# Optimization experiments

Hardware: AMD Instinct MI355X
Metric: run time of the kernel (lower is better)

## Reference

```python
import jax, jax.numpy as jnp
import numpy as np

# Model dims (match init_kwargs)
E, D, H, K = 8, 512, 1024, 2   # num_experts, input/output dim, hidden dim, top_k
B, S = 4, 2048                 # batch, seq_len


def setup_inputs() -> dict:
    key = jax.random.key(0)
    ks = jax.random.split(key, 5)
    sd = lambda fan: np.float32(1.0 / np.sqrt(fan))
    return {
        "x": jax.random.normal(ks[0], (B, S, D), jnp.float32),
        "gate_w": jax.random.normal(ks[1], (D, E), jnp.float32) * sd(D),
        "gate_b": jnp.zeros((E,), jnp.float32),
        "w1": jax.random.normal(ks[2], (E, D, H), jnp.float32) * sd(D),
        "b1": jnp.zeros((E, H), jnp.float32),
        "w2": jax.random.normal(ks[3], (E, H, D), jnp.float32) * sd(H),
        "b2": jnp.zeros((E, D), jnp.float32),
    }


def reference(x, gate_w, gate_b, w1, b1, w2, b2):
    # x: [B, S, D]
    Bb, Ss, Dd = x.shape
    xf = x.reshape(-1, Dd)                              # [N, D], N = B*S

    # Router: softmax over experts, top-k, renormalize selected weights
    logits = xf @ gate_w + gate_b                        # [N, E]
    probs = jax.nn.softmax(logits, axis=-1)              # [N, E]
    top_w, top_i = jax.lax.top_k(probs, K)               # [N, K]
    top_w = top_w / top_w.sum(axis=-1, keepdims=True)

    # Per-token combine weight for each expert (0 if not routed).
    onehot = jax.nn.one_hot(top_i, E, dtype=probs.dtype)  # [N, K, E]
    combine = jnp.einsum("nke,nk->ne", onehot, top_w)     # [N, E]

    # Expert MLPs. Dropout is inactive at inference (identity).
    # h: [E, N, H]; GELU exact (torch nn.GELU default uses erf)
    h = jax.nn.gelu(jnp.einsum("nd,edh->enh", xf, w1) + b1[:, None, :],
                    approximate=False)
    y = jnp.einsum("enh,ehd->end", h, w2) + b2[:, None, :]  # [E, N, D]

    # Weighted combine: tokens not routed to expert e have combine[:, e] == 0.
    out = jnp.einsum("end,ne->nd", y, combine).reshape(Bb, Ss, Dd)
    return out, probs.reshape(Bb, Ss, E)
```

## Files before the change

### kernel.cpp

```cpp
#include <hip/hip_runtime.h>
#include <stdint.h>

#define N_TOK 8192
#define DIM   512
#define HID   1024
#define NE    8
#define NSLOT 16384
#define MAXSLOT 17408

typedef __attribute__((ext_vector_type(8))) short short8;
typedef __attribute__((ext_vector_type(4))) float f32x4;

#define W1T_OFF  0ull
#define W2T_OFF  8388608ull
#define H_OFF    16777216ull
#define Y_OFF    52428800ull
#define XBF_OFF  52428800ull
#define TOPI_OFF 70254592ull
#define TOPW_OFF 70320128ull
#define SLOT_OFF 70385664ull
#define ROWS_OFF 70451200ull
#define RW_OFF   70520832ull
#define CNT_OFF  70590464ull

__device__ __forceinline__ unsigned int f2bfu(float f) {
  union { float f; unsigned int i; } v; v.f = f;
  unsigned int u = v.i;
  return (u + 0x7FFFu + ((u >> 16) & 1u)) >> 16;
}
__device__ __forceinline__ float bf2f(unsigned int u) {
  union { unsigned int i; float f; } v; v.i = (u & 0xFFFFu) << 16; return v.f;
}
__device__ __forceinline__ float gelu_f(float x) {
  float x2 = x * x;
  float u = x * (1.59576912f + 0.07135481f * x2);
  float ez = __expf(-u);
  return x * __builtin_amdgcn_rcpf(1.0f + ez);
}
__device__ __forceinline__ void async16(void* lds, const void* g) {
  __builtin_amdgcn_global_load_lds(
      (const __attribute__((address_space(1))) unsigned int*)g,
      (__attribute__((address_space(3))) unsigned int*)lds, 16, 0, 0);
}

__global__ __launch_bounds__(256) void k_prep(
    const float* __restrict__ w1, const float* __restrict__ w2,
    unsigned short* __restrict__ w1t, unsigned short* __restrict__ w2t,
    const float* __restrict__ x, const float* __restrict__ gw,
    const float* __restrict__ gb, float* __restrict__ probs_out,
    int2* __restrict__ topi, float2* __restrict__ topw,
    unsigned short* __restrict__ xbf) {
  __shared__ unsigned short tile[64][68];
  int tid = threadIdx.x;
  if (blockIdx.x < 2048) {
    int b = blockIdx.x;
    const float* src; unsigned short* dst; int R, C;
    if (b < 1024) { int e = b >> 7; int t = b & 127;
      src = w1 + (size_t)e * 524288; dst = w1t + (size_t)e * 524288; R = 512; C = 1024;
      int tr = t >> 4, tc = t & 15;
      src += (size_t)tr * 64 * C + tc * 64; dst += (size_t)tc * 64 * R + tr * 64;
    } else { b -= 1024; int e = b >> 7; int t = b & 127;
      src = w2 + (size_t)e * 524288; dst = w2t + (size_t)e * 524288; R = 1024; C = 512;
      int tr = t >> 3, tc = t & 7;
      src += (size_t)tr * 64 * C + tc * 64; dst += (size_t)tc * 64 * R + tr * 64;
    }
#pragma unroll
    for (int i = 0; i < 4; ++i) {
      int l = i * 256 + tid;
      int r = l >> 4, c4 = (l & 15) << 2;
      float4 v = *(const float4*)(src + (size_t)r * C + c4);
      tile[r][c4 + 0] = (unsigned short)f2bfu(v.x);
      tile[r][c4 + 1] = (unsigned short)f2bfu(v.y);
      tile[r][c4 + 2] = (unsigned short)f2bfu(v.z);
      tile[r][c4 + 3] = (unsigned short)f2bfu(v.w);
    }
    __syncthreads();
#pragma unroll
    for (int i = 0; i < 2; ++i) {
      int l = i * 256 + tid;
      int rr = l >> 3, c8 = (l & 7) << 3;
      ushort4 a, b2v;
      a.x = tile[c8 + 0][rr]; a.y = tile[c8 + 1][rr];
      a.z = tile[c8 + 2][rr]; a.w = tile[c8 + 3][rr];
      b2v.x = tile[c8 + 4][rr]; b2v.y = tile[c8 + 5][rr];
      b2v.z = tile[c8 + 6][rr]; b2v.w = tile[c8 + 7][rr];
      uint4 pk;
      pk.x = (unsigned int)a.x | ((unsigned int)a.y << 16);
      pk.y = (unsigned int)a.z | ((unsigned int)a.w << 16);
      pk.z = (unsigned int)b2v.x | ((unsigned int)b2v.y << 16);
      pk.w = (unsigned int)b2v.z | ((unsigned int)b2v.w << 16);
      *(uint4*)(dst + (size_t)rr * R + c8) = pk;
    }
  } else {
    int wave = tid >> 6, lane = tid & 63;
    int n = (blockIdx.x - 2048) * 4 + wave;
    const float4* xr = (const float4*)(x + (size_t)n * DIM);
    float4 x0 = xr[lane * 2], x1 = xr[lane * 2 + 1];
    float xf[8] = {x0.x, x0.y, x0.z, x0.w, x1.x, x1.y, x1.z, x1.w};
    uint4 pa;
    pa.x = f2bfu(xf[0]) | (f2bfu(xf[1]) << 16);
    pa.y = f2bfu(xf[2]) | (f2bfu(xf[3]) << 16);
    pa.z = f2bfu(xf[4]) | (f2bfu(xf[5]) << 16);
    pa.w = f2bfu(xf[6]) | (f2bfu(xf[7]) << 16);
    *(uint4*)(xbf + (size_t)n * DIM + lane * 8) = pa;
    float acc[8] = {0.f,0.f,0.f,0.f,0.f,0.f,0.f,0.f};
    const float4* gwr = (const float4*)gw;
#pragma unroll
    for (int j = 0; j < 8; ++j) {
      int d = lane * 8 + j;
      float4 g0 = gwr[d * 2], g1 = gwr[d * 2 + 1];
      acc[0] += xf[j] * g0.x; acc[1] += xf[j] * g0.y; acc[2] += xf[j] * g0.z; acc[3] += xf[j] * g0.w;
      acc[4] += xf[j] * g1.x; acc[5] += xf[j] * g1.y; acc[6] += xf[j] * g1.z; acc[7] += xf[j] * g1.w;
    }
#pragma unroll
    for (int o = 1; o < 64; o <<= 1)
#pragma unroll
      for (int e = 0; e < 8; ++e) acc[e] += __shfl_xor(acc[e], o, 64);
    float p[8], mx = -1e30f, s = 0.f;
#pragma unroll
    for (int e = 0; e < 8; ++e) { p[e] = acc[e] + gb[e]; mx = fmaxf(mx, p[e]); }
#pragma unroll
    for (int e = 0; e < 8; ++e) { p[e] = __expf(p[e] - mx); s += p[e]; }
    float inv = 1.f / s;
#pragma unroll
    for (int e = 0; e < 8; ++e) p[e] *= inv;
    if (lane < 8) probs_out[(size_t)n * NE + lane] = p[lane];
    if (lane == 0) {
      int i0 = 0; float v0 = p[0];
#pragma unroll
      for (int e = 1; e < 8; ++e) if (p[e] > v0) { v0 = p[e]; i0 = e; }
      int i1 = -1; float v1 = -1.f;
#pragma unroll
      for (int e = 0; e < 8; ++e) if (e != i0 && p[e] > v1) { v1 = p[e]; i1 = e; }
      float sw = 1.f / (v0 + v1);
      topi[n] = make_int2(i0, i1);
      topw[n] = make_float2(v0 * sw, v1 * sw);
    }
  }
}

__global__ __launch_bounds__(1024) void k_countassign(
    const int2* __restrict__ topi, const float2* __restrict__ topw,
    int* __restrict__ meta, int* __restrict__ rows, float* __restrict__ rw,
    int* __restrict__ slot_of) {
  __shared__ int ch[32][8];
  __shared__ int tot[8], poff_s[9], tiles_s[8];
  __shared__ int sm_off[1024 * 8];
  int t = threadIdx.x, g = t >> 5;
  if (t < 256) ((int*)ch)[t] = 0;
  __syncthreads();
  int2 te[8]; float2 tw[8];
  int c[8] = {0,0,0,0,0,0,0,0};
  int base_tok = t * 8;
#pragma unroll
  for (int i = 0; i < 8; ++i) {
    te[i] = topi[base_tok + i];
    tw[i] = topw[base_tok + i];
#pragma unroll
    for (int k = 0; k < 8; ++k) c[k] += (te[i].x == k) + (te[i].y == k);
  }
#pragma unroll
  for (int k = 0; k < 8; ++k) if (c[k]) atomicAdd(&ch[g][k], c[k]);
#pragma unroll
  for (int k = 0; k < 8; ++k) {
    int s = c[k];
#pragma unroll
    for (int d = 1; d < 32; d <<= 1) {
      int u = __shfl_up(s, d, 32);
      if ((t & 31) >= d) s += u;
    }
    sm_off[t * 8 + k] = s - c[k];
  }
  __syncthreads();
  if (t < 8) {
    int a = 0;
#pragma unroll
    for (int b = 0; b < 32; ++b) { int v = ch[b][t]; ch[b][t] = a; a += v; }
    tot[t] = a; meta[t] = a;
  }
  __syncthreads();
  if (t == 0) {
    int a = 0, ts = 0;
#pragma unroll
    for (int e = 0; e < 8; ++e) {
      int tiles = (tot[e] + 127) >> 7;
      poff_s[e] = a; tiles_s[e] = tiles;
      meta[16 + e] = a; meta[32 + e] = ts;
      a += tiles << 7; ts += tiles;
    }
    poff_s[8] = a; meta[24] = a; meta[40] = ts;
  }
  __syncthreads();
#pragma unroll
  for (int i = 0; i < 8; ++i) {
    int n = base_tok + i;
    int e0 = te[i].x, e1 = te[i].y;
    int o0 = sm_off[t * 8 + e0]++;
    int s0 = poff_s[e0] + ch[g][e0] + o0;
    int o1 = sm_off[t * 8 + e1]++;
    int s1 = poff_s[e1] + ch[g][e1] + o1;
    rows[s0] = n; rw[s0] = tw[i].x; slot_of[2 * n] = s0;
    rows[s1] = n; rw[s1] = tw[i].y; slot_of[2 * n + 1] = s1;
  }
#pragma unroll
  for (int e = 0; e < 8; ++e) {
    int padn = (tiles_s[e] << 7) - tot[e];
    if (t < padn) {
      int s = poff_s[e] + tot[e] + t;
      rows[s] = 0; rw[s] = 0.f;
    }
  }
}

__global__ __launch_bounds__(256) void k_gemm1(
    const unsigned short* __restrict__ xbf, const unsigned short* __restrict__ w1t,
    const float* __restrict__ b1, const int* __restrict__ meta,
    const int* __restrict__ rows, unsigned short* __restrict__ h) {
  int lin = blockIdx.x;
  int xcd = lin & 7, j = lin >> 3;
  int t = xcd * 17 + (j >> 3);
  int nt = j & 7;
  if (t >= meta[40]) return;
  int e = 0;
#pragma unroll
  for (int i = 1; i < 8; ++i) if (t >= meta[32 + i]) e = i;
  int mt = t - meta[32 + e];
  int row0 = meta[16 + e] + (mt << 7);
  __shared__ __align__(16) unsigned short As[2][8192];
  __shared__ __align__(16) unsigned short Bs[2][8192];
  int tid = threadIdx.x;
  int wave = tid >> 6, lane = tid & 63;
  int wr = wave & 1, wc = wave >> 1;
  int ml = lane & 15, q = lane >> 4;
  f32x4 acc[4][4] = {};
  const unsigned short* bBase = w1t + (size_t)e * HID * DIM + (size_t)(nt * 128) * DIM;

  const unsigned short* ga[4]; const unsigned short* gb[4];
#pragma unroll
  for (int jj = 0; jj < 4; ++jj) {
    int s = jj * 256 + tid;
    int ks = s >> 9, r = (s >> 2) & 127, cs = s & 3;
    int col = ks * 32 + ((cs ^ ((r >> 1) & 3)) << 3);
    ga[jj] = xbf + (size_t)rows[row0 + r] * DIM + col;
    gb[jj] = bBase + (size_t)r * DIM + col;
  }

#define STAGE1(buf, k0) do { \
    _Pragma("unroll") \
    for (int jj = 0; jj < 4; ++jj) { \
      int dst = (jj * 256 + wave * 64) * 8; \
      async16(&As[buf][dst], ga[jj] + (k0)); \
      async16(&Bs[buf][dst], gb[jj] + (k0)); \
    } \
  } while (0)

  STAGE1(0, 0);
  __syncthreads();

  for (int k0 = 0; k0 < DIM; k0 += 64) {
    int cur = (k0 >> 6) & 1, nxt = cur ^ 1;
    if (k0 + 64 < DIM) STAGE1(nxt, k0 + 64);
#pragma unroll
    for (int ks = 0; ks < 2; ++ks) {
      short8 tf[4], wf[4];
#pragma unroll
      for (int am = 0; am < 4; ++am) {
        int ra = wr * 64 + am * 16 + ml;
        tf[am] = *(const short8*)&As[cur][ks * 4096 + (ra * 4 + (q ^ ((ra >> 1) & 3))) * 8];
      }
#pragma unroll
      for (int an = 0; an < 4; ++an) {
        int rb = wc * 64 + an * 16 + ml;
        wf[an] = *(const short8*)&Bs[cur][ks * 4096 + (rb * 4 + (q ^ ((rb >> 1) & 3))) * 8];
      }
#pragma unroll
      for (int an = 0; an < 4; ++an)
#pragma unroll
        for (int am = 0; am < 4; ++am)
          acc[an][am] = __builtin_amdgcn_mfma_f32_16x16x32_bf16(wf[an], tf[am], acc[an][am], 0, 0, 0);
    }
    __syncthreads();
  }
#undef STAGE1

#pragma unroll
  for (int am = 0; am < 4; ++am) {
    int slot_r = row0 + wr * 64 + am * 16 + ml;
    unsigned short* hrow = h + (size_t)slot_r * HID;
#pragma unroll
    for (int an = 0; an < 4; ++an) {
      int colb = nt * 128 + wc * 64 + an * 16 + q * 4;
      float4 bias = *(const float4*)&b1[e * HID + colb];
      f32x4 v = acc[an][am];
      float g0 = gelu_f(v[0] + bias.x);
      float g1 = gelu_f(v[1] + bias.y);
      float g2 = gelu_f(v[2] + bias.z);
      float g3 = gelu_f(v[3] + bias.w);
      uint2 pk;
      pk.x = f2bfu(g0) | (f2bfu(g1) << 16);
      pk.y = f2bfu(g2) | (f2bfu(g3) << 16);
      *(uint2*)(hrow + colb) = pk;
    }
  }
}

__global__ __launch_bounds__(256) void k_gemm2(
    const unsigned short* __restrict__ h, const unsigned short* __restrict__ w2t,
    const float* __restrict__ b2, const int* __restrict__ meta,
    const float* __restrict__ rw, unsigned short* __restrict__ y) {
  int lin = blockIdx.x;
  int xcd = lin & 7, j = lin >> 3;
  int t = xcd * 17 + (j >> 2);
  int nt = j & 3;
  if (t >= meta[40]) return;
  int e = 0;
#pragma unroll
  for (int i = 1; i < 8; ++i) if (t >= meta[32 + i]) e = i;
  int mt = t - meta[32 + e];
  int row0 = meta[16 + e] + (mt << 7);
  __shared__ __align__(16) unsigned short As[2][8192];
  __shared__ __align__(16) unsigned short Bs[2][8192];
  int tid = threadIdx.x;
  int wave = tid >> 6, lane = tid & 63;
  int wr = wave & 1, wc = wave >> 1;
  int ml = lane & 15, q = lane >> 4;
  f32x4 acc[4][4] = {};
  const unsigned short* aBase = h + (size_t)row0 * HID;
  const unsigned short* bBase = w2t + (size_t)e * DIM * HID + (size_t)(nt * 128) * HID;

  const unsigned short* ga[4]; const unsigned short* gb[4];
#pragma unroll
  for (int jj = 0; jj < 4; ++jj) {
    int s = jj * 256 + tid;
    int ks = s >> 9, r = (s >> 2) & 127, cs = s & 3;
    int col = ks * 32 + ((cs ^ ((r >> 1) & 3)) << 3);
    ga[jj] = aBase + (size_t)r * HID + col;
    gb[jj] = bBase + (size_t)r * HID + col;
  }

#define STAGE2(buf, k0) do { \
    _Pragma("unroll") \
    for (int jj = 0; jj < 4; ++jj) { \
      int dst = (jj * 256 + wave * 64) * 8; \
      async16(&As[buf][dst], ga[jj] + (k0)); \
      async16(&Bs[buf][dst], gb[jj] + (k0)); \
    } \
  } while (0)

  STAGE2(0, 0);
  __syncthreads();

  for (int k0 = 0; k0 < HID; k0 += 64) {
    int cur = (k0 >> 6) & 1, nxt = cur ^ 1;
    if (k0 + 64 < HID) STAGE2(nxt, k0 + 64);
#pragma unroll
    for (int ks = 0; ks < 2; ++ks) {
      short8 tf[4], wf[4];
#pragma unroll
      for (int am = 0; am < 4; ++am) {
        int ra = wr * 64 + am * 16 + ml;
        tf[am] = *(const short8*)&As[cur][ks * 4096 + (ra * 4 + (q ^ ((ra >> 1) & 3))) * 8];
      }
#pragma unroll
      for (int an = 0; an < 4; ++an) {
        int rb = wc * 64 + an * 16 + ml;
        wf[an] = *(const short8*)&Bs[cur][ks * 4096 + (rb * 4 + (q ^ ((rb >> 1) & 3))) * 8];
      }
#pragma unroll
      for (int an = 0; an < 4; ++an)
#pragma unroll
        for (int am = 0; am < 4; ++am)
          acc[an][am] = __builtin_amdgcn_mfma_f32_16x16x32_bf16(wf[an], tf[am], acc[an][am], 0, 0, 0);
    }
    __syncthreads();
  }
#undef STAGE2

#pragma unroll
  for (int am = 0; am < 4; ++am) {
    int slot_r = row0 + wr * 64 + am * 16 + ml;
    float w = rw[slot_r];
    unsigned short* yrow = y + (size_t)slot_r * DIM;
#pragma unroll
    for (int an = 0; an < 4; ++an) {
      int colb = nt * 128 + wc * 64 + an * 16 + q * 4;
      float4 bias = *(const float4*)&b2[e * DIM + colb];
      f32x4 v = acc[an][am];
      uint2 pk;
      pk.x = f2bfu((v[0] + bias.x) * w) | (f2bfu((v[1] + bias.y) * w) << 16);
      pk.y = f2bfu((v[2] + bias.z) * w) | (f2bfu((v[3] + bias.w) * w) << 16);
      *(uint2*)(yrow + colb) = pk;
    }
  }
}

__global__ __launch_bounds__(256) void k_combine(
    const unsigned short* __restrict__ y, const int* __restrict__ slot_of,
    float* __restrict__ out) {
  int t = blockIdx.x * 256 + threadIdx.x;
  int n = t >> 6, c = (t & 63) << 3;
  int s0 = slot_of[2 * n], s1 = slot_of[2 * n + 1];
  uint4 u0 = *(const uint4*)(y + (size_t)s0 * DIM + c);
  uint4 u1 = *(const uint4*)(y + (size_t)s1 * DIM + c);
  float4 o0, o1;
  o0.x = bf2f(u0.x) + bf2f(u1.x); o0.y = bf2f(u0.x >> 16) + bf2f(u1.x >> 16);
  o0.z = bf2f(u0.y) + bf2f(u1.y); o0.w = bf2f(u0.y >> 16) + bf2f(u1.y >> 16);
  o1.x = bf2f(u0.z) + bf2f(u1.z); o1.y = bf2f(u0.z >> 16) + bf2f(u1.z >> 16);
  o1.z = bf2f(u0.w) + bf2f(u1.w); o1.w = bf2f(u0.w >> 16) + bf2f(u1.w >> 16);
  *(float4*)(out + (size_t)n * DIM + c) = o0;
  *(float4*)(out + (size_t)n * DIM + c + 4) = o1;
}

extern "C" void kernel_launch(void* const* d_in, const int* in_sizes, int n_in,
                              void* d_out, int out_size, void* d_ws, size_t ws_size,
                              hipStream_t stream) {
  const float* x  = (const float*)d_in[0];
  const float* gw = (const float*)d_in[1];
  const float* gb = (const float*)d_in[2];
  const float* w1 = (const float*)d_in[3];
  const float* b1 = (const float*)d_in[4];
  const float* w2 = (const float*)d_in[5];
  const float* b2 = (const float*)d_in[6];
  float* out = (float*)d_out;
  char* ws = (char*)d_ws;

  unsigned short* w1t = (unsigned short*)(ws + W1T_OFF);
  unsigned short* w2t = (unsigned short*)(ws + W2T_OFF);
  unsigned short* h   = (unsigned short*)(ws + H_OFF);
  unsigned short* y   = (unsigned short*)(ws + Y_OFF);
  unsigned short* xbf = (unsigned short*)(ws + XBF_OFF);
  int2*   topi    = (int2*)(ws + TOPI_OFF);
  float2* topw    = (float2*)(ws + TOPW_OFF);
  int*    slot_of = (int*)(ws + SLOT_OFF);
  int*    rows    = (int*)(ws + ROWS_OFF);
  float*  rw      = (float*)(ws + RW_OFF);
  int*    meta    = (int*)(ws + CNT_OFF);
  float*  probs   = out + (size_t)N_TOK * DIM;

  k_prep       <<<dim3(4096), dim3(256),  0, stream>>>(w1, w2, w1t, w2t,
                                                       x, gw, gb, probs, topi, topw, xbf);
  k_countassign<<<dim3(1),    dim3(1024), 0, stream>>>(topi, topw, meta, rows, rw, slot_of);
  k_gemm1      <<<dim3(1088), dim3(256),  0, stream>>>(xbf, w1t, b1, meta, rows, h);
  k_gemm2      <<<dim3(544),  dim3(256),  0, stream>>>(h, w2t, b2, meta, rw, y);
  k_combine    <<<dim3(2048), dim3(256),  0, stream>>>(y, slot_of, out);
}
```

Baseline: 214.2 us.

## Enlarge expert GEMM M-tiles to 256 rows with 8 waves and K-step 32

Both expert GEMMs now use 256-row M tiles (per-expert padding to 256) with 512-thread blocks of 8 waves arranged 4x2, while the K step per stage drops from 64 to 32. Weight tiles are reused across more token rows, cutting global weight traffic, and LDS per block shrinks on the B side. The tradeoffs are more padding waste per expert, fewer blocks (less parallelism on a large GPU), and twice as many barriers per K loop. Workspace offsets are enlarged to fit the bigger padded slot count.

```diff
diff --git a/kernel.cpp b/kernel.cpp
--- a/kernel.cpp
+++ b/kernel.cpp
@@ -6,7 +6,7 @@
 #define HID   1024
 #define NE    8
 #define NSLOT 16384
-#define MAXSLOT 17408
+#define MAXSLOT 18432
 
 typedef __attribute__((ext_vector_type(8))) short short8;
 typedef __attribute__((ext_vector_type(4))) float f32x4;
@@ -14,14 +14,14 @@
 #define W1T_OFF  0ull
 #define W2T_OFF  8388608ull
 #define H_OFF    16777216ull
-#define Y_OFF    52428800ull
-#define XBF_OFF  52428800ull
-#define TOPI_OFF 70254592ull
-#define TOPW_OFF 70320128ull
-#define SLOT_OFF 70385664ull
-#define ROWS_OFF 70451200ull
-#define RW_OFF   70520832ull
-#define CNT_OFF  70590464ull
+#define Y_OFF    54525952ull
+#define XBF_OFF  54525952ull
+#define TOPI_OFF 73400320ull
+#define TOPW_OFF 73465856ull
+#define SLOT_OFF 73531392ull
+#define ROWS_OFF 73596928ull
+#define RW_OFF   73670656ull
+#define CNT_OFF  73744384ull
 
 __device__ __forceinline__ unsigned int f2bfu(float f) {
   union { float f; unsigned int i; } v; v.f = f;
@@ -183,10 +183,10 @@
     int a = 0, ts = 0;
 #pragma unroll
     for (int e = 0; e < 8; ++e) {
-      int tiles = (tot[e] + 127) >> 7;
+      int tiles = (tot[e] + 255) >> 8;
       poff_s[e] = a; tiles_s[e] = tiles;
       meta[16 + e] = a; meta[32 + e] = ts;
-      a += tiles << 7; ts += tiles;
+      a += tiles << 8; ts += tiles;
     }
     poff_s[8] = a; meta[24] = a; meta[40] = ts;
   }
@@ -204,7 +204,7 @@
   }
 #pragma unroll
   for (int e = 0; e < 8; ++e) {
-    int padn = (tiles_s[e] << 7) - tot[e];
+    int padn = (tiles_s[e] << 8) - tot[e];
     if (t < padn) {
       int s = poff_s[e] + tot[e] + t;
       rows[s] = 0; rw[s] = 0.f;
@@ -212,66 +212,65 @@
   }
 }
 
-__global__ __launch_bounds__(256) void k_gemm1(
+__global__ __launch_bounds__(512, 4) void k_gemm1(
     const unsigned short* __restrict__ xbf, const unsigned short* __restrict__ w1t,
     const float* __restrict__ b1, const int* __restrict__ meta,
     const int* __restrict__ rows, unsigned short* __restrict__ h) {
   int lin = blockIdx.x;
   int xcd = lin & 7, j = lin >> 3;
-  int t = xcd * 17 + (j >> 3);
+  int t = xcd * 9 + (j >> 3);
   int nt = j & 7;
   if (t >= meta[40]) return;
   int e = 0;
 #pragma unroll
   for (int i = 1; i < 8; ++i) if (t >= meta[32 + i]) e = i;
   int mt = t - meta[32 + e];
-  int row0 = meta[16 + e] + (mt << 7);
+  int row0 = meta[16 + e] + (mt << 8);
   __shared__ __align__(16) unsigned short As[2][8192];
-  __shared__ __align__(16) unsigned short Bs[2][8192];
+  __shared__ __align__(16) unsigned short Bs[2][4096];
   int tid = threadIdx.x;
   int wave = tid >> 6, lane = tid & 63;
-  int wr = wave & 1, wc = wave >> 1;
+  int wr = wave & 3, wc = wave >> 2;
   int ml = lane & 15, q = lane >> 4;
   f32x4 acc[4][4] = {};
   const unsigned short* bBase = w1t + (size_t)e * HID * DIM + (size_t)(nt * 128) * DIM;
 
-  const unsigned short* ga[4]; const unsigned short* gb[4];
-#pragma unroll
-  for (int jj = 0; jj < 4; ++jj) {
-    int s = jj * 256 + tid;
-    int ks = s >> 9, r = (s >> 2) & 127, cs = s & 3;
-    int col = ks * 32 + ((cs ^ ((r >> 1) & 3)) << 3);
-    ga[jj] = xbf + (size_t)rows[row0 + r] * DIM + col;
-    gb[jj] = bBase + (size_t)r * DIM + col;
-  }
+  const unsigned short *ga0, *ga1, *gbp;
+  {
+    int s0 = tid;        int r0 = s0 >> 2; int c0 = ((s0 & 3) ^ ((r0 >> 1) & 3)) << 3;
+    ga0 = xbf + (size_t)rows[row0 + r0] * DIM + c0;
+    int s1 = 512 + tid;  int r1 = s1 >> 2; int c1 = ((s1 & 3) ^ ((r1 >> 1) & 3)) << 3;
+    ga1 = xbf + (size_t)rows[row0 + r1] * DIM + c1;
+    int sb = tid;        int rb = sb >> 2; int cb = ((sb & 3) ^ ((rb >> 1) & 3)) << 3;
+    gbp = bBase + (size_t)rb * DIM + cb;
+  }
+  int la0 = (wave * 64) * 8;
+  int la1 = (512 + wave * 64) * 8;
+  int lb  = (wave * 64) * 8;
 
 #define STAGE1(buf, k0) do { \
-    _Pragma("unroll") \
-    for (int jj = 0; jj < 4; ++jj) { \
-      int dst = (jj * 256 + wave * 64) * 8; \
-      async16(&As[buf][dst], ga[jj] + (k0)); \
-      async16(&Bs[buf][dst], gb[jj] + (k0)); \
-    } \
+    async16(&As[buf][la0], ga0 + (k0)); \
+    async16(&As[buf][la1], ga1 + (k0)); \
+    async16(&Bs[buf][lb],  gbp + (k0)); \
   } while (0)
 
   STAGE1(0, 0);
   __syncthreads();
 
-  for (int k0 = 0; k0 < DIM; k0 += 64) {
-    int cur = (k0 >> 6) & 1, nxt = cur ^ 1;
-    if (k0 + 64 < DIM) STAGE1(nxt, k0 + 64);
-#pragma unroll
-    for (int ks = 0; ks < 2; ++ks) {
+  for (int k0 = 0; k0 < DIM; k0 += 32) {
+    int cur = (k0 >> 5) & 1, nxt = cur ^ 1;
+    if (k0 + 32 < DIM) STAGE1(nxt, k0 + 32);
+    {
       short8 tf[4], wf[4];
 #pragma unroll
       for (int am = 0; am < 4; ++am) {
         int ra = wr * 64 + am * 16 + ml;
-        tf[am] = *(const short8*)&As[cur][ks * 4096 + (ra * 4 + (q ^ ((ra >> 1) & 3))) * 8];
+        tf[am] = *(const short8*)&As[cur][(ra * 4 + (q ^ ((ra >> 1) & 3))) * 8];
       }
 #pragma unroll
       for (int an = 0; an < 4; ++an) {
         int rb = wc * 64 + an * 16 + ml;
-        wf[an] = *(const short8*)&Bs[cur][ks * 4096 + (rb * 4 + (q ^ ((rb >> 1) & 3))) * 8];
+        wf[an] = *(const short8*)&Bs[cur][(rb * 4 + (q ^ ((rb >> 1) & 3))) * 8];
       }
 #pragma unroll
       for (int an = 0; an < 4; ++an)
@@ -304,67 +303,66 @@
   }
 }
 
-__global__ __launch_bounds__(256) void k_gemm2(
+__global__ __launch_bounds__(512, 4) void k_gemm2(
     const unsigned short* __restrict__ h, const unsigned short* __restrict__ w2t,
     const float* __restrict__ b2, const int* __restrict__ meta,
     const float* __restrict__ rw, unsigned short* __restrict__ y) {
   int lin = blockIdx.x;
   int xcd = lin & 7, j = lin >> 3;
-  int t = xcd * 17 + (j >> 2);
+  int t = xcd * 9 + (j >> 2);
   int nt = j & 3;
   if (t >= meta[40]) return;
   int e = 0;
 #pragma unroll
   for (int i = 1; i < 8; ++i) if (t >= meta[32 + i]) e = i;
   int mt = t - meta[32 + e];
-  int row0 = meta[16 + e] + (mt << 7);
+  int row0 = meta[16 + e] + (mt << 8);
   __shared__ __align__(16) unsigned short As[2][8192];
-  __shared__ __align__(16) unsigned short Bs[2][8192];
+  __shared__ __align__(16) unsigned short Bs[2][4096];
   int tid = threadIdx.x;
   int wave = tid >> 6, lane = tid & 63;
-  int wr = wave & 1, wc = wave >> 1;
+  int wr = wave & 3, wc = wave >> 2;
   int ml = lane & 15, q = lane >> 4;
   f32x4 acc[4][4] = {};
   const unsigned short* aBase = h + (size_t)row0 * HID;
   const unsigned short* bBase = w2t + (size_t)e * DIM * HID + (size_t)(nt * 128) * HID;
 
-  const unsigned short* ga[4]; const unsigned short* gb[4];
-#pragma unroll
-  for (int jj = 0; jj < 4; ++jj) {
-    int s = jj * 256 + tid;
-    int ks = s >> 9, r = (s >> 2) & 127, cs = s & 3;
-    int col = ks * 32 + ((cs ^ ((r >> 1) & 3)) << 3);
-    ga[jj] = aBase + (size_t)r * HID + col;
-    gb[jj] = bBase + (size_t)r * HID + col;
-  }
+  const unsigned short *ga0, *ga1, *gbp;
+  {
+    int s0 = tid;        int r0 = s0 >> 2; int c0 = ((s0 & 3) ^ ((r0 >> 1) & 3)) << 3;
+    ga0 = aBase + (size_t)r0 * HID + c0;
+    int s1 = 512 + tid;  int r1 = s1 >> 2; int c1 = ((s1 & 3) ^ ((r1 >> 1) & 3)) << 3;
+    ga1 = aBase + (size_t)r1 * HID + c1;
+    int sb = tid;        int rb = sb >> 2; int cb = ((sb & 3) ^ ((rb >> 1) & 3)) << 3;
+    gbp = bBase + (size_t)rb * HID + cb;
+  }
+  int la0 = (wave * 64) * 8;
+  int la1 = (512 + wave * 64) * 8;
+  int lb  = (wave * 64) * 8;
 
 #define STAGE2(buf, k0) do { \
-    _Pragma("unroll") \
-    for (int jj = 0; jj < 4; ++jj) { \
-      int dst = (jj * 256 + wave * 64) * 8; \
-      async16(&As[buf][dst], ga[jj] + (k0)); \
-      async16(&Bs[buf][dst], gb[jj] + (k0)); \
-    } \
+    async16(&As[buf][la0], ga0 + (k0)); \
+    async16(&As[buf][la1], ga1 + (k0)); \
+    async16(&Bs[buf][lb],  gbp + (k0)); \
   } while (0)
 
   STAGE2(0, 0);
   __syncthreads();
 
-  for (int k0 = 0; k0 < HID; k0 += 64) {
-    int cur = (k0 >> 6) & 1, nxt = cur ^ 1;
-    if (k0 + 64 < HID) STAGE2(nxt, k0 + 64);
-#pragma unroll
-    for (int ks = 0; ks < 2; ++ks) {
+  for (int k0 = 0; k0 < HID; k0 += 32) {
+    int cur = (k0 >> 5) & 1, nxt = cur ^ 1;
+    if (k0 + 32 < HID) STAGE2(nxt, k0 + 32);
+    {
       short8 tf[4], wf[4];
 #pragma unroll
       for (int am = 0; am < 4; ++am) {
         int ra = wr * 64 + am * 16 + ml;
-        tf[am] = *(const short8*)&As[cur][ks * 4096 + (ra * 4 + (q ^ ((ra >> 1) & 3))) * 8];
+        tf[am] = *(const short8*)&As[cur][(ra * 4 + (q ^ ((ra >> 1) & 3))) * 8];
       }
 #pragma unroll
       for (int an = 0; an < 4; ++an) {
         int rb = wc * 64 + an * 16 + ml;
-        wf[an] = *(const short8*)&Bs[cur][ks * 4096 + (rb * 4 + (q ^ ((rb >> 1) & 3))) * 8];
+        wf[an] = *(const short8*)&Bs[cur][(rb * 4 + (q ^ ((rb >> 1) & 3))) * 8];
       }
 #pragma unroll
       for (int an = 0; an < 4; ++an)
@@ -440,7 +438,7 @@
   k_prep       <<<dim3(4096), dim3(256),  0, stream>>>(w1, w2, w1t, w2t,
                                                        x, gw, gb, probs, topi, topw, xbf);
   k_countassign<<<dim3(1),    dim3(1024), 0, stream>>>(topi, topw, meta, rows, rw, slot_of);
-  k_gemm1      <<<dim3(1088), dim3(256),  0, stream>>>(xbf, w1t, b1, meta, rows, h);
-  k_gemm2      <<<dim3(544),  dim3(256),  0, stream>>>(h, w2t, b2, meta, rw, y);
+  k_gemm1      <<<dim3(576),  dim3(512),  0, stream>>>(xbf, w1t, b1, meta, rows, h);
+  k_gemm2      <<<dim3(288),  dim3(512),  0, stream>>>(h, w2t, b2, meta, rw, y);
   k_combine    <<<dim3(2048), dim3(256),  0, stream>>>(y, slot_of, out);
 }
```

Measured after the change: 215.3 us. Within noise of the previous version (+0.5%).

## Triple-buffer GEMM K-loop with 32-wide tiles and explicit vmcnt waits

Applied to the files above, without the earlier changes.

Both expert GEMM kernels move from a double-buffered 64-wide K step with __syncthreads to a three-stage ring of 32-wide K tiles. Two loads stay in flight, and s_waitcnt vmcnt plus a single s_barrier per step replace the full sync. The aim is to hide global-load latency behind MFMA work and to cut LDS use per block (48KB instead of 64KB), which may allow more resident blocks. The cost is twice as many barriers per K, and correctness now depends on the hand-set vmcnt counts matching the async load count.

```diff
diff --git a/kernel.cpp b/kernel.cpp
--- a/kernel.cpp
+++ b/kernel.cpp
@@ -226,8 +226,8 @@
   for (int i = 1; i < 8; ++i) if (t >= meta[32 + i]) e = i;
   int mt = t - meta[32 + e];
   int row0 = meta[16 + e] + (mt << 7);
-  __shared__ __align__(16) unsigned short As[2][8192];
-  __shared__ __align__(16) unsigned short Bs[2][8192];
+  __shared__ __align__(16) unsigned short As[3][4096];
+  __shared__ __align__(16) unsigned short Bs[3][4096];
   int tid = threadIdx.x;
   int wave = tid >> 6, lane = tid & 63;
   int wr = wave & 1, wc = wave >> 1;
@@ -235,51 +235,50 @@
   f32x4 acc[4][4] = {};
   const unsigned short* bBase = w1t + (size_t)e * HID * DIM + (size_t)(nt * 128) * DIM;
 
-  const unsigned short* ga[4]; const unsigned short* gb[4];
-#pragma unroll
-  for (int jj = 0; jj < 4; ++jj) {
+  const unsigned short* ga[2]; const unsigned short* gb[2];
+#pragma unroll
+  for (int jj = 0; jj < 2; ++jj) {
     int s = jj * 256 + tid;
-    int ks = s >> 9, r = (s >> 2) & 127, cs = s & 3;
-    int col = ks * 32 + ((cs ^ ((r >> 1) & 3)) << 3);
-    ga[jj] = xbf + (size_t)rows[row0 + r] * DIM + col;
-    gb[jj] = bBase + (size_t)r * DIM + col;
-  }
-
-#define STAGE1(buf, k0) do { \
+    int r = s >> 2;
+    int cg = ((s & 3) ^ ((r >> 1) & 3)) << 3;
+    ga[jj] = xbf + (size_t)rows[row0 + r] * DIM + cg;
+    gb[jj] = bBase + (size_t)r * DIM + cg;
+  }
+  int ldst = (wave * 64) * 8;
+
+#define STAGE1(buf, kt) do { \
     _Pragma("unroll") \
-    for (int jj = 0; jj < 4; ++jj) { \
-      int dst = (jj * 256 + wave * 64) * 8; \
-      async16(&As[buf][dst], ga[jj] + (k0)); \
-      async16(&Bs[buf][dst], gb[jj] + (k0)); \
+    for (int jj = 0; jj < 2; ++jj) { \
+      async16(&As[buf][jj * 2048 + ldst], ga[jj] + (kt) * 32); \
+      async16(&Bs[buf][jj * 2048 + ldst], gb[jj] + (kt) * 32); \
     } \
   } while (0)
 
-  STAGE1(0, 0);
-  __syncthreads();
-
-  for (int k0 = 0; k0 < DIM; k0 += 64) {
-    int cur = (k0 >> 6) & 1, nxt = cur ^ 1;
-    if (k0 + 64 < DIM) STAGE1(nxt, k0 + 64);
-#pragma unroll
-    for (int ks = 0; ks < 2; ++ks) {
-      short8 tf[4], wf[4];
-#pragma unroll
-      for (int am = 0; am < 4; ++am) {
-        int ra = wr * 64 + am * 16 + ml;
-        tf[am] = *(const short8*)&As[cur][ks * 4096 + (ra * 4 + (q ^ ((ra >> 1) & 3))) * 8];
-      }
-#pragma unroll
-      for (int an = 0; an < 4; ++an) {
-        int rb = wc * 64 + an * 16 + ml;
-        wf[an] = *(const short8*)&Bs[cur][ks * 4096 + (rb * 4 + (q ^ ((rb >> 1) & 3))) * 8];
-      }
-#pragma unroll
-      for (int an = 0; an < 4; ++an)
-#pragma unroll
-        for (int am = 0; am < 4; ++am)
-          acc[an][am] = __builtin_amdgcn_mfma_f32_16x16x32_bf16(wf[an], tf[am], acc[an][am], 0, 0, 0);
-    }
-    __syncthreads();
+  STAGE1(0, 0); STAGE1(1, 1);
+
+#pragma unroll
+  for (int kt = 0; kt < 16; ++kt) {
+    if (kt < 15) { asm volatile("s_waitcnt vmcnt(4)" ::: "memory"); }
+    else         { asm volatile("s_waitcnt vmcnt(0)" ::: "memory"); }
+    __builtin_amdgcn_s_barrier();
+    if (kt < 14) STAGE1((kt + 2) % 3, kt + 2);
+    int cur = kt % 3;
+    short8 tf[4], wf[4];
+#pragma unroll
+    for (int am = 0; am < 4; ++am) {
+      int ra = wr * 64 + am * 16 + ml;
+      tf[am] = *(const short8*)&As[cur][(ra * 4 + (q ^ ((ra >> 1) & 3))) * 8];
+    }
+#pragma unroll
+    for (int an = 0; an < 4; ++an) {
+      int rb = wc * 64 + an * 16 + ml;
+      wf[an] = *(const short8*)&Bs[cur][(rb * 4 + (q ^ ((rb >> 1) & 3))) * 8];
+    }
+#pragma unroll
+    for (int an = 0; an < 4; ++an)
+#pragma unroll
+      for (int am = 0; am < 4; ++am)
+        acc[an][am] = __builtin_amdgcn_mfma_f32_16x16x32_bf16(wf[an], tf[am], acc[an][am], 0, 0, 0);
   }
 #undef STAGE1
 
@@ -318,8 +317,8 @@
   for (int i = 1; i < 8; ++i) if (t >= meta[32 + i]) e = i;
   int mt = t - meta[32 + e];
   int row0 = meta[16 + e] + (mt << 7);
-  __shared__ __align__(16) unsigned short As[2][8192];
-  __shared__ __align__(16) unsigned short Bs[2][8192];
+  __shared__ __align__(16) unsigned short As[3][4096];
+  __shared__ __align__(16) unsigned short Bs[3][4096];
   int tid = threadIdx.x;
   int wave = tid >> 6, lane = tid & 63;
   int wr = wave & 1, wc = wave >> 1;
@@ -328,51 +327,50 @@
   const unsigned short* aBase = h + (size_t)row0 * HID;
   const unsigned short* bBase = w2t + (size_t)e * DIM * HID + (size_t)(nt * 128) * HID;
 
-  const unsigned short* ga[4]; const unsigned short* gb[4];
-#pragma unroll
-  for (int jj = 0; jj < 4; ++jj) {
+  const unsigned short* ga[2]; const unsigned short* gb[2];
+#pragma unroll
+  for (int jj = 0; jj < 2; ++jj) {
     int s = jj * 256 + tid;
-    int ks = s >> 9, r = (s >> 2) & 127, cs = s & 3;
-    int col = ks * 32 + ((cs ^ ((r >> 1) & 3)) << 3);
-    ga[jj] = aBase + (size_t)r * HID + col;
-    gb[jj] = bBase + (size_t)r * HID + col;
-  }
-
-#define STAGE2(buf, k0) do { \
+    int r = s >> 2;
+    int cg = ((s & 3) ^ ((r >> 1) & 3)) << 3;
+    ga[jj] = aBase + (size_t)r * HID + cg;
+    gb[jj] = bBase + (size_t)r * HID + cg;
+  }
+  int ldst = (wave * 64) * 8;
+
+#define STAGE2(buf, kt) do { \
     _Pragma("unroll") \
-    for (int jj = 0; jj < 4; ++jj) { \
-      int dst = (jj * 256 + wave * 64) * 8; \
-      async16(&As[buf][dst], ga[jj] + (k0)); \
-      async16(&Bs[buf][dst], gb[jj] + (k0)); \
+    for (int jj = 0; jj < 2; ++jj) { \
+      async16(&As[buf][jj * 2048 + ldst], ga[jj] + (kt) * 32); \
+      async16(&Bs[buf][jj * 2048 + ldst], gb[jj] + (kt) * 32); \
     } \
   } while (0)
 
-  STAGE2(0, 0);
-  __syncthreads();
-
-  for (int k0 = 0; k0 < HID; k0 += 64) {
-    int cur = (k0 >> 6) & 1, nxt = cur ^ 1;
-    if (k0 + 64 < HID) STAGE2(nxt, k0 + 64);
-#pragma unroll
-    for (int ks = 0; ks < 2; ++ks) {
-      short8 tf[4], wf[4];
-#pragma unroll
-      for (int am = 0; am < 4; ++am) {
-        int ra = wr * 64 + am * 16 + ml;
-        tf[am] = *(const short8*)&As[cur][ks * 4096 + (ra * 4 + (q ^ ((ra >> 1) & 3))) * 8];
-      }
-#pragma unroll
-      for (int an = 0; an < 4; ++an) {
-        int rb = wc * 64 + an * 16 + ml;
-        wf[an] = *(const short8*)&Bs[cur][ks * 4096 + (rb * 4 + (q ^ ((rb >> 1) & 3))) * 8];
-      }
-#pragma unroll
-      for (int an = 0; an < 4; ++an)
-#pragma unroll
-        for (int am = 0; am < 4; ++am)
-          acc[an][am] = __builtin_amdgcn_mfma_f32_16x16x32_bf16(wf[an], tf[am], acc[an][am], 0, 0, 0);
-    }
-    __syncthreads();
+  STAGE2(0, 0); STAGE2(1, 1);
+
+#pragma unroll
+  for (int kt = 0; kt < 32; ++kt) {
+    if (kt < 31) { asm volatile("s_waitcnt vmcnt(4)" ::: "memory"); }
+    else         { asm volatile("s_waitcnt vmcnt(0)" ::: "memory"); }
+    __builtin_amdgcn_s_barrier();
+    if (kt < 30) STAGE2((kt + 2) % 3, kt + 2);
+    int cur = kt % 3;
+    short8 tf[4], wf[4];
+#pragma unroll
+    for (int am = 0; am < 4; ++am) {
+      int ra = wr * 64 + am * 16 + ml;
+      tf[am] = *(const short8*)&As[cur][(ra * 4 + (q ^ ((ra >> 1) & 3))) * 8];
+    }
+#pragma unroll
+    for (int an = 0; an < 4; ++an) {
+      int rb = wc * 64 + an * 16 + ml;
+      wf[an] = *(const short8*)&Bs[cur][(rb * 4 + (q ^ ((rb >> 1) & 3))) * 8];
+    }
+#pragma unroll
+    for (int an = 0; an < 4; ++an)
+#pragma unroll
+      for (int am = 0; am < 4; ++am)
+        acc[an][am] = __builtin_amdgcn_mfma_f32_16x16x32_bf16(wf[an], tf[am], acc[an][am], 0, 0, 0);
   }
 #undef STAGE2
 
```

Result: faster. 207.6 us (-3.1%).
